# Kernel optimization log

Hardware: AMD Instinct MI355X
Metric: run time of the kernel (lower is better)

## Reference

```python
import jax, jax.numpy as jnp
import numpy as np

D_MODEL = 1024
H = 16
D_K = 64
D_V = 64
NEG_INF = -1e9
LN_EPS = 1e-5


def setup_inputs() -> dict:
    key = jax.random.key(0)
    ks = jax.random.split(key, 7)
    B, S = 4, 2048
    scale = 1.0 / np.sqrt(D_MODEL)
    return {
        "Q": jax.random.normal(ks[0], (B, S, D_MODEL), jnp.float32),
        "K": jax.random.normal(ks[1], (B, S, D_MODEL), jnp.float32),
        "V": jax.random.normal(ks[2], (B, S, D_MODEL), jnp.float32),
        "W_Q": jax.random.normal(ks[3], (D_MODEL, D_K * H), jnp.float32) * scale,
        "W_K": jax.random.normal(ks[4], (D_MODEL, D_K * H), jnp.float32) * scale,
        "W_V": jax.random.normal(ks[5], (D_MODEL, D_V * H), jnp.float32) * scale,
        "W_O": jax.random.normal(ks[6], (D_V * H, D_MODEL), jnp.float32) * scale,
        "ln_gamma": jnp.ones((D_MODEL,), jnp.float32),
        "ln_beta": jnp.zeros((D_MODEL,), jnp.float32),
    }


def reference(Q, K, V, W_Q, W_K, W_V, W_O, ln_gamma, ln_beta):
    B, Lq, _ = Q.shape
    Lk = K.shape[1]
    # projections, split into heads: [B, H, L, d]
    Qh = (Q @ W_Q).reshape(B, Lq, H, D_K).transpose(0, 2, 1, 3)
    Kh = (K @ W_K).reshape(B, Lk, H, D_K).transpose(0, 2, 1, 3)
    Vh = (V @ W_V).reshape(B, Lk, H, D_V).transpose(0, 2, 1, 3)
    # scaled dot-product scores [B, H, Lq, Lk]
    scores = jnp.einsum("bhqd,bhkd->bhqk", Qh, Kh) / jnp.sqrt(jnp.float32(D_K))
    # causal mask: upper triangle (excl. diagonal) gets -1e9 added
    mask = jnp.triu(jnp.full((Lq, Lk), NEG_INF, jnp.float32), k=1)
    scores = scores + mask
    attn = jax.nn.softmax(scores, axis=-1)
    ctx = jnp.einsum("bhqk,bhkd->bhqd", attn, Vh)
    ctx = ctx.transpose(0, 2, 1, 3).reshape(B, Lq, H * D_V)
    out = ctx @ W_O
    # residual + layernorm
    x = Q + out
    mu = jnp.mean(x, axis=-1, keepdims=True)
    var = jnp.mean(jnp.square(x - mu), axis=-1, keepdims=True)
    return (x - mu) * jax.lax.rsqrt(var + LN_EPS) * ln_gamma + ln_beta
```

## Files before the change

### kernel.cpp

```cpp
#include <hip/hip_runtime.h>
#include <cstdint>
#include <cstddef>

#define DM  1024
#define SEQ 2048
#define BATCH 4
#define NH  16
#define DH  64
#define QKVS 3072

typedef __bf16 bf16_t;
typedef __bf16 bf16x8 __attribute__((ext_vector_type(8)));
typedef __bf16 bf16x4 __attribute__((ext_vector_type(4)));
typedef float  f32x4  __attribute__((ext_vector_type(4)));

#define MFMA16(a, b, c) __builtin_amdgcn_mfma_f32_16x16x32_bf16((a), (b), (c), 0, 0, 0)

#define CS 0.18033688f

#define ASYNC_COPY16(gsrc, ldst)                                                   \
  __builtin_amdgcn_global_load_lds(                                                \
      (__attribute__((address_space(1))) void*)(gsrc),                             \
      (__attribute__((address_space(3))) void*)(ldst), 16, 0, 0)

#define NCVT (3 * BATCH * SEQ * DM / 4 / 256)

__global__ __launch_bounds__(256) void prep_kernel(const float* __restrict__ Q,
                                                   const float* __restrict__ K,
                                                   const float* __restrict__ V,
                                                   const float* __restrict__ W0,
                                                   const float* __restrict__ W1,
                                                   const float* __restrict__ W2,
                                                   const float* __restrict__ W3,
                                                   bf16_t* __restrict__ Qb,
                                                   bf16_t* __restrict__ Kb,
                                                   bf16_t* __restrict__ Vb,
                                                   bf16_t* __restrict__ WTall) {
  __shared__ float tile[32][33];
  const int bid = blockIdx.x;
  if (bid < NCVT) {
    const int n4 = BATCH * SEQ * DM / 4;
    int i = bid * 256 + threadIdx.x;
    const float* src; bf16_t* dst; int j;
    if (i < n4)           { src = Q; dst = Qb; j = i; }
    else if (i < 2 * n4)  { src = K; dst = Kb; j = i - n4; }
    else                  { src = V; dst = Vb; j = i - 2 * n4; }
    float4 v = ((const float4*)src)[j];
    bf16x4 o;
    o[0] = (bf16_t)v.x; o[1] = (bf16_t)v.y; o[2] = (bf16_t)v.z; o[3] = (bf16_t)v.w;
    *(bf16x4*)(dst + (size_t)j * 4) = o;
    return;
  }
  const int wb = bid - NCVT;
  const int widx = wb >> 10, wid = wb & 1023;
  const float* W = (widx == 0) ? W0 : (widx == 1) ? W1 : (widx == 2) ? W2 : W3;
  bf16_t* WT = WTall + (size_t)widx * DM * DM;
  const int bn = wid & 31, bk = wid >> 5;
  const int tx = threadIdx.x & 31, ty = threadIdx.x >> 5;
#pragma unroll
  for (int r = 0; r < 4; ++r)
    tile[ty + r * 8][tx] = W[(size_t)(bk * 32 + ty + r * 8) * DM + bn * 32 + tx];
  __syncthreads();
#pragma unroll
  for (int r = 0; r < 4; ++r)
    WT[(size_t)(bn * 32 + ty + r * 8) * DM + bk * 32 + tx] = (bf16_t)tile[tx][ty + r * 8];
}

template <typename OutT>
__global__ __launch_bounds__(256) void gemm_bt_kernel(const bf16_t* __restrict__ A0,
                                                      const bf16_t* __restrict__ A1,
                                                      const bf16_t* __restrict__ A2,
                                                      const bf16_t* __restrict__ BT,
                                                      OutT* __restrict__ C,
                                                      int K, int ldc,
                                                      float qscale, int qcols) {
  __shared__ bf16_t As[128 * 32];
  __shared__ bf16_t Bs[128 * 32];
  const int tid = threadIdx.x;
  const int wv = tid >> 6, lane = tid & 63;
  const int lo = lane & 15, quad = lane >> 4;

  const int bid = blockIdx.x;
  const int xcd = bid & 7;
  const int rid = bid >> 3;
  const int m0 = (xcd * 8 + (rid & 7)) * 128;
  const int n0 = (rid >> 3) * 128;
  const int wm = wv & 1, wn = wv >> 1;

  const bf16_t* A = (n0 < 1024) ? A0 : (n0 < 2048) ? A1 : A2;
  const float sc = (n0 < qcols) ? qscale : 1.0f;

  f32x4 acc[4][4] = {};

  const int srow = wv * 32 + (lane >> 2);
  const int scol = (lane & 3) * 8;
  const bf16_t* Ag = A + (size_t)(m0 + srow) * K + scol;
  const bf16_t* Bg = BT + (size_t)(n0 + srow) * K + scol;
  bf16_t* Asl = As + (wv * 32) * 32;
  bf16_t* Bsl = Bs + (wv * 32) * 32;

  for (int k0 = 0; k0 < K; k0 += 32) {
    __syncthreads();
    ASYNC_COPY16(Ag + k0, Asl);
    ASYNC_COPY16(Ag + k0 + (size_t)16 * K, Asl + 16 * 32);
    ASYNC_COPY16(Bg + k0, Bsl);
    ASYNC_COPY16(Bg + k0 + (size_t)16 * K, Bsl + 16 * 32);
    __syncthreads();

    bf16x8 af[4], bfr[4];
#pragma unroll
    for (int t = 0; t < 4; ++t) {
      af[t]  = *(const bf16x8*)(As + (wm * 64 + t * 16 + lo) * 32 + quad * 8);
      bfr[t] = *(const bf16x8*)(Bs + (wn * 64 + t * 16 + lo) * 32 + quad * 8);
    }
#pragma unroll
    for (int mt = 0; mt < 4; ++mt)
#pragma unroll
      for (int nt = 0; nt < 4; ++nt)
        acc[mt][nt] = MFMA16(af[mt], bfr[nt], acc[mt][nt]);
  }

#pragma unroll
  for (int mt = 0; mt < 4; ++mt)
#pragma unroll
    for (int nt = 0; nt < 4; ++nt)
#pragma unroll
      for (int r = 0; r < 4; ++r) {
        const int m = m0 + wm * 64 + mt * 16 + quad * 4 + r;
        const int n = n0 + wn * 64 + nt * 16 + lo;
        C[(size_t)m * ldc + n] = (OutT)(acc[mt][nt][r] * sc);
      }
}

__global__ __launch_bounds__(256) void vtrans_kernel(const bf16_t* __restrict__ QKV,
                                                     bf16_t* __restrict__ Vt) {
  __shared__ bf16_t tile[64][72];
  const int bh = blockIdx.x >> 5, jt = blockIdx.x & 31;
  const int b = bh >> 4, h = bh & 15;
  const bf16_t* src = QKV + ((size_t)(b * SEQ + jt * 64)) * QKVS + 2048 + h * DH;
  const int jr = threadIdx.x >> 3, c8 = (threadIdx.x & 7) * 8;
#pragma unroll
  for (int it = 0; it < 2; ++it) {
    const int j = jr + it * 32;
    *(bf16x8*)(&tile[j][c8]) = *(const bf16x8*)(src + (size_t)j * QKVS + c8);
  }
  __syncthreads();
  const int d = threadIdx.x >> 2, jc = (threadIdx.x & 3) * 16;
  bf16x8 o0, o1;
#pragma unroll
  for (int u = 0; u < 8; ++u) { o0[u] = tile[jc + u][d]; o1[u] = tile[jc + 8 + u][d]; }
  bf16_t* dst = Vt + ((size_t)(bh * 64 + d)) * SEQ + jt * 64 + jc;
  *(bf16x8*)(dst) = o0;
  *(bf16x8*)(dst + 8) = o1;
}

__global__ __launch_bounds__(256) void attn_kernel(const bf16_t* __restrict__ QKV,
                                                   const bf16_t* __restrict__ Vt,
                                                   bf16_t* __restrict__ ctx) {
  __shared__ bf16_t Ks[2][64 * 64];
  __shared__ bf16_t Vs[2][64 * 64];
  __shared__ bf16_t Ps[4][16 * 64];
  const int tid = threadIdx.x;
  const int wv = tid >> 6, lane = tid & 63;
  const int lo = lane & 15, quad = lane >> 4;
  const int bh = blockIdx.x & 63;
  const int pid = blockIdx.x >> 6;
  const int b = bh >> 4, h = bh & 15;

  const bf16_t* Qg = QKV + ((size_t)b * SEQ) * QKVS + h * DH;
  const bf16_t* Kg = QKV + ((size_t)b * SEQ) * QKVS + 1024 + h * DH;
  const bf16_t* Vg = Vt + ((size_t)(bh * DH)) * SEQ;

  const int U0 = wv * 128 + lane, U1 = U0 + 64;
  const int r0 = U0 >> 3, cg0 = (U0 & 7) ^ (r0 & 7);
  const int r1 = U1 >> 3, cg1 = (U1 & 7) ^ (r1 & 7);

  bf16_t* Pw = &Ps[wv][0];

  for (int half = 0; half < 2; ++half) {
    const int qblk = half ? (31 - pid) : pid;
    const int qw0 = qblk * 64 + wv * 16;
    const int qg = qw0 + lo;

    const bf16_t* Qb = Qg + ((size_t)(qw0 + lo)) * QKVS + quad * 8;
    const bf16x8 aQ0 = *(const bf16x8*)(Qb);
    const bf16x8 aQ1 = *(const bf16x8*)(Qb + 32);

    f32x4 O[4] = {};
    float l_run = 0.0f;

    __syncthreads();
    ASYNC_COPY16(Kg + (size_t)r0 * QKVS + cg0 * 8, Ks[0] + (wv * 2 + 0) * 512);
    ASYNC_COPY16(Kg + (size_t)r1 * QKVS + cg1 * 8, Ks[0] + (wv * 2 + 1) * 512);
    ASYNC_COPY16(Vg + (size_t)r0 * SEQ + cg0 * 8, Vs[0] + (wv * 2 + 0) * 512);
    ASYNC_COPY16(Vg + (size_t)r1 * SEQ + cg1 * 8, Vs[0] + (wv * 2 + 1) * 512);

    for (int jt = 0; jt <= qblk; ++jt) {
      const int cur = jt & 1;
      __syncthreads();
      if (jt < qblk) {
        const int j1 = (jt + 1) * 64;
        ASYNC_COPY16(Kg + (size_t)(j1 + r0) * QKVS + cg0 * 8, Ks[cur ^ 1] + (wv * 2 + 0) * 512);
        ASYNC_COPY16(Kg + (size_t)(j1 + r1) * QKVS + cg1 * 8, Ks[cur ^ 1] + (wv * 2 + 1) * 512);
        ASYNC_COPY16(Vg + (size_t)r0 * SEQ + j1 + cg0 * 8, Vs[cur ^ 1] + (wv * 2 + 0) * 512);
        ASYNC_COPY16(Vg + (size_t)r1 * SEQ + j1 + cg1 * 8, Vs[cur ^ 1] + (wv * 2 + 1) * 512);
      }

      const int j0 = jt * 64;
      f32x4 st[4];
#pragma unroll
      for (int mt = 0; mt < 4; ++mt) {
        const int row = mt * 16 + lo;
        const bf16x8 k0 = *(const bf16x8*)(Ks[cur] + row * 64 + ((quad ^ (row & 7)) * 8));
        const bf16x8 k1 = *(const bf16x8*)(Ks[cur] + row * 64 + (((4 + quad) ^ (row & 7)) * 8));
        f32x4 s = {};
        s = MFMA16(k0, aQ0, s);
        s = MFMA16(k1, aQ1, s);
        st[mt] = s;
      }

      float lsum = 0.0f;
      const bool diag = (jt == qblk);
#pragma unroll
      for (int mt = 0; mt < 4; ++mt) {
        bf16x4 pk;
#pragma unroll
        for (int r = 0; r < 4; ++r) {
          float s = st[mt][r];
          if (diag && (j0 + mt * 16 + quad * 4 + r > qg)) s = -1e30f;
          const float p = __builtin_amdgcn_exp2f(s);
          lsum += p;
          pk[r] = (bf16_t)p;
        }
        const int sp = (mt * 2 + (quad >> 1)) ^ (lo & 7);
        *(bf16x4*)(Pw + lo * 64 + sp * 8 + (quad & 1) * 4) = pk;
      }
      lsum += __shfl_xor(lsum, 16);
      lsum += __shfl_xor(lsum, 32);
      l_run += lsum;

      __asm__ volatile("s_waitcnt lgkmcnt(0)" ::: "memory");
      const bf16x8 p0 = *(const bf16x8*)(Pw + lo * 64 + ((quad ^ (lo & 7)) * 8));
      const bf16x8 p1 = *(const bf16x8*)(Pw + lo * 64 + (((4 + quad) ^ (lo & 7)) * 8));
#pragma unroll
      for (int nt = 0; nt < 4; ++nt) {
        const int row = nt * 16 + lo;
        const bf16x8 v0 = *(const bf16x8*)(Vs[cur] + row * 64 + ((quad ^ (row & 7)) * 8));
        const bf16x8 v1 = *(const bf16x8*)(Vs[cur] + row * 64 + (((4 + quad) ^ (row & 7)) * 8));
        O[nt] = MFMA16(p0, v0, O[nt]);
        O[nt] = MFMA16(p1, v1, O[nt]);
      }
    }

    float inv[4];
#pragma unroll
    for (int r = 0; r < 4; ++r) inv[r] = 1.0f / __shfl(l_run, quad * 4 + r);
    bf16_t* outp = ctx + ((size_t)(b * SEQ + qw0 + quad * 4)) * DM + h * DH + lo;
#pragma unroll
    for (int r = 0; r < 4; ++r)
#pragma unroll
      for (int nt = 0; nt < 4; ++nt)
        outp[(size_t)r * DM + nt * 16] = (bf16_t)(O[nt][r] * inv[r]);
  }
}

__global__ __launch_bounds__(256) void ln_kernel(const float* __restrict__ Qin,
                                                 const bf16_t* __restrict__ Y,
                                                 const float* __restrict__ gamma,
                                                 const float* __restrict__ beta,
                                                 float* __restrict__ out) {
  const int row = blockIdx.x, t = threadIdx.x;
  const float4 a = ((const float4*)(Qin + (size_t)row * DM))[t];
  const bf16x4 yv = ((const bf16x4*)(Y + (size_t)row * DM))[t];
  const float x0 = a.x + (float)yv[0], x1 = a.y + (float)yv[1];
  const float x2 = a.z + (float)yv[2], x3 = a.w + (float)yv[3];
  float s  = x0 + x1 + x2 + x3;
  float ss = x0 * x0 + x1 * x1 + x2 * x2 + x3 * x3;
#pragma unroll
  for (int off = 1; off < 64; off <<= 1) { s += __shfl_xor(s, off); ss += __shfl_xor(ss, off); }
  __shared__ float red[8];
  const int wv = t >> 6, lane = t & 63;
  if (lane == 0) { red[wv * 2] = s; red[wv * 2 + 1] = ss; }
  __syncthreads();
  s  = red[0] + red[2] + red[4] + red[6];
  ss = red[1] + red[3] + red[5] + red[7];
  const float mu  = s * (1.0f / DM);
  const float var = ss * (1.0f / DM) - mu * mu;
  const float rstd = rsqrtf(var + 1e-5f);
  const float4 g  = ((const float4*)gamma)[t];
  const float4 be = ((const float4*)beta)[t];
  float4 o;
  o.x = (x0 - mu) * rstd * g.x + be.x;
  o.y = (x1 - mu) * rstd * g.y + be.y;
  o.z = (x2 - mu) * rstd * g.z + be.z;
  o.w = (x3 - mu) * rstd * g.w + be.w;
  ((float4*)(out + (size_t)row * DM))[t] = o;
}

extern "C" void kernel_launch(void* const* d_in, const int* in_sizes, int n_in,
                              void* d_out, int out_size, void* d_ws, size_t ws_size,
                              hipStream_t stream) {
  const float* Q     = (const float*)d_in[0];
  const float* K     = (const float*)d_in[1];
  const float* V     = (const float*)d_in[2];
  const float* W_Q   = (const float*)d_in[3];
  const float* W_K   = (const float*)d_in[4];
  const float* W_V   = (const float*)d_in[5];
  const float* W_O   = (const float*)d_in[6];
  const float* gamma = (const float*)d_in[7];
  const float* beta  = (const float*)d_in[8];
  float* out = (float*)d_out;

  char* ws = (char*)d_ws;
  const size_t SZB = (size_t)BATCH * SEQ * DM * 2;
  const size_t WTB = (size_t)DM * DM * 2;
  bf16_t* Qb    = (bf16_t*)(ws);
  bf16_t* Kb    = (bf16_t*)(ws + SZB);
  bf16_t* Vb    = (bf16_t*)(ws + 2 * SZB);
  bf16_t* Yb    = (bf16_t*)(ws);
  bf16_t* WTall = (bf16_t*)(ws + 3 * SZB);
  char* p2 = ws + 3 * SZB + 4 * WTB;
  bf16_t* QKV = (bf16_t*)(p2);
  bf16_t* Vtr = (bf16_t*)(p2 + 3 * SZB);
  bf16_t* ctx = (bf16_t*)(p2 + 4 * SZB);

  prep_kernel<<<NCVT + 4096, 256, 0, stream>>>(Q, K, V, W_Q, W_K, W_V, W_O,
                                               Qb, Kb, Vb, WTall);

  gemm_bt_kernel<bf16_t><<<(QKVS / 128) * (BATCH * SEQ / 128), 256, 0, stream>>>(
      Qb, Kb, Vb, WTall, QKV, DM, QKVS, CS, 1024);

  vtrans_kernel<<<BATCH * NH * (SEQ / 64), 256, 0, stream>>>(QKV, Vtr);

  attn_kernel<<<64 * 16, 256, 0, stream>>>(QKV, Vtr, ctx);

  gemm_bt_kernel<bf16_t><<<(DM / 128) * (BATCH * SEQ / 128), 256, 0, stream>>>(
      ctx, ctx, ctx, WTall + (size_t)3 * DM * DM, Yb, DM, DM, 1.0f, 0);
  ln_kernel<<<BATCH * SEQ, 256, 0, stream>>>(Q, Yb, gamma, beta, out);
}
```

Measured before the change: 337.8 us.

## Fuse V transpose into QKV GEMM epilogue and double-buffer GEMM LDS loads

The QKV projection GEMM now writes the V columns straight into the transposed per-head layout through an LDS-staged, swizzled epilogue. This removes the separate vtrans kernel and the round trip of V through global memory, and the QKV buffer shrinks to Q and K only. The GEMM main loop also double-buffers its A/B tiles in LDS, so the next K-slice is prefetched while MFMAs run, cutting one barrier per iteration. The cost is twice the LDS per block, which may lower occupancy, plus extra epilogue complexity.

Result: faster. 316.3 us (-6.4%).

```diff
diff --git a/kernel.cpp b/kernel.cpp
--- a/kernel.cpp
+++ b/kernel.cpp
@@ -7,7 +7,7 @@
 #define BATCH 4
 #define NH  16
 #define DH  64
-#define QKVS 3072
+#define QKS 2048
 
 typedef __bf16 bf16_t;
 typedef __bf16 bf16x8 __attribute__((ext_vector_type(8)));
@@ -66,16 +66,15 @@
     WT[(size_t)(bn * 32 + ty + r * 8) * DM + bk * 32 + tx] = (bf16_t)tile[tx][ty + r * 8];
 }
 
-template <typename OutT>
 __global__ __launch_bounds__(256) void gemm_bt_kernel(const bf16_t* __restrict__ A0,
                                                       const bf16_t* __restrict__ A1,
                                                       const bf16_t* __restrict__ A2,
                                                       const bf16_t* __restrict__ BT,
-                                                      OutT* __restrict__ C,
+                                                      bf16_t* __restrict__ C,
+                                                      bf16_t* __restrict__ Vtr,
                                                       int K, int ldc,
                                                       float qscale, int qcols) {
-  __shared__ bf16_t As[128 * 32];
-  __shared__ bf16_t Bs[128 * 32];
+  __shared__ bf16_t Sh[4][128 * 32];
   const int tid = threadIdx.x;
   const int wv = tid >> 6, lane = tid & 63;
   const int lo = lane & 15, quad = lane >> 4;
@@ -96,22 +95,30 @@
   const int scol = (lane & 3) * 8;
   const bf16_t* Ag = A + (size_t)(m0 + srow) * K + scol;
   const bf16_t* Bg = BT + (size_t)(n0 + srow) * K + scol;
-  bf16_t* Asl = As + (wv * 32) * 32;
-  bf16_t* Bsl = Bs + (wv * 32) * 32;
-
-  for (int k0 = 0; k0 < K; k0 += 32) {
+  const int lds_off = (wv * 32) * 32;
+
+  ASYNC_COPY16(Ag, Sh[0] + lds_off);
+  ASYNC_COPY16(Ag + (size_t)16 * K, Sh[0] + lds_off + 16 * 32);
+  ASYNC_COPY16(Bg, Sh[2] + lds_off);
+  ASYNC_COPY16(Bg + (size_t)16 * K, Sh[2] + lds_off + 16 * 32);
+
+  const int kiters = K >> 5;
+  for (int ki = 0; ki < kiters; ++ki) {
+    const int cur = ki & 1;
     __syncthreads();
-    ASYNC_COPY16(Ag + k0, Asl);
-    ASYNC_COPY16(Ag + k0 + (size_t)16 * K, Asl + 16 * 32);
-    ASYNC_COPY16(Bg + k0, Bsl);
-    ASYNC_COPY16(Bg + k0 + (size_t)16 * K, Bsl + 16 * 32);
-    __syncthreads();
+    if (ki + 1 < kiters) {
+      const int k1 = (ki + 1) << 5;
+      ASYNC_COPY16(Ag + k1, Sh[cur ^ 1] + lds_off);
+      ASYNC_COPY16(Ag + k1 + (size_t)16 * K, Sh[cur ^ 1] + lds_off + 16 * 32);
+      ASYNC_COPY16(Bg + k1, Sh[2 + (cur ^ 1)] + lds_off);
+      ASYNC_COPY16(Bg + k1 + (size_t)16 * K, Sh[2 + (cur ^ 1)] + lds_off + 16 * 32);
+    }
 
     bf16x8 af[4], bfr[4];
 #pragma unroll
     for (int t = 0; t < 4; ++t) {
-      af[t]  = *(const bf16x8*)(As + (wm * 64 + t * 16 + lo) * 32 + quad * 8);
-      bfr[t] = *(const bf16x8*)(Bs + (wn * 64 + t * 16 + lo) * 32 + quad * 8);
+      af[t]  = *(const bf16x8*)(Sh[cur] + (wm * 64 + t * 16 + lo) * 32 + quad * 8);
+      bfr[t] = *(const bf16x8*)(Sh[2 + cur] + (wn * 64 + t * 16 + lo) * 32 + quad * 8);
     }
 #pragma unroll
     for (int mt = 0; mt < 4; ++mt)
@@ -120,6 +127,38 @@
         acc[mt][nt] = MFMA16(af[mt], bfr[nt], acc[mt][nt]);
   }
 
+  __syncthreads();
+
+  if (Vtr != nullptr && n0 >= 2048) {
+    bf16_t* Tw = &Sh[wv][0];
+#pragma unroll
+    for (int nt = 0; nt < 4; ++nt) {
+      const int row = nt * 16 + lo;
+#pragma unroll
+      for (int mt = 0; mt < 4; ++mt) {
+        const int cb = mt * 16 + quad * 4;
+        bf16x4 pk;
+#pragma unroll
+        for (int r = 0; r < 4; ++r) pk[r] = (bf16_t)acc[mt][nt][r];
+        *(bf16x4*)(Tw + row * 64 + (((cb >> 3) ^ (row & 7)) * 8) + (cb & 7)) = pk;
+      }
+    }
+    __asm__ volatile("s_waitcnt lgkmcnt(0)" ::: "memory");
+    const int h  = ((n0 - 2048) >> 6) + wn;
+    const int mg = m0 + wm * 64;
+    const int b  = mg >> 11;
+    const int s0 = mg & (SEQ - 1);
+    const int dr = lane >> 3, ck = lane & 7;
+    bf16_t* vbase = Vtr + ((size_t)((b * NH + h) * DH)) * SEQ + s0;
+#pragma unroll
+    for (int pass = 0; pass < 8; ++pass) {
+      const int d = pass * 8 + dr;
+      const bf16x8 vv = *(const bf16x8*)(Tw + d * 64 + ((ck ^ (d & 7)) * 8));
+      *(bf16x8*)(vbase + (size_t)d * SEQ + ck * 8) = vv;
+    }
+    return;
+  }
+
 #pragma unroll
   for (int mt = 0; mt < 4; ++mt)
 #pragma unroll
@@ -128,30 +167,8 @@
       for (int r = 0; r < 4; ++r) {
         const int m = m0 + wm * 64 + mt * 16 + quad * 4 + r;
         const int n = n0 + wn * 64 + nt * 16 + lo;
-        C[(size_t)m * ldc + n] = (OutT)(acc[mt][nt][r] * sc);
-      }
-}
-
-__global__ __launch_bounds__(256) void vtrans_kernel(const bf16_t* __restrict__ QKV,
-                                                     bf16_t* __restrict__ Vt) {
-  __shared__ bf16_t tile[64][72];
-  const int bh = blockIdx.x >> 5, jt = blockIdx.x & 31;
-  const int b = bh >> 4, h = bh & 15;
-  const bf16_t* src = QKV + ((size_t)(b * SEQ + jt * 64)) * QKVS + 2048 + h * DH;
-  const int jr = threadIdx.x >> 3, c8 = (threadIdx.x & 7) * 8;
-#pragma unroll
-  for (int it = 0; it < 2; ++it) {
-    const int j = jr + it * 32;
-    *(bf16x8*)(&tile[j][c8]) = *(const bf16x8*)(src + (size_t)j * QKVS + c8);
-  }
-  __syncthreads();
-  const int d = threadIdx.x >> 2, jc = (threadIdx.x & 3) * 16;
-  bf16x8 o0, o1;
-#pragma unroll
-  for (int u = 0; u < 8; ++u) { o0[u] = tile[jc + u][d]; o1[u] = tile[jc + 8 + u][d]; }
-  bf16_t* dst = Vt + ((size_t)(bh * 64 + d)) * SEQ + jt * 64 + jc;
-  *(bf16x8*)(dst) = o0;
-  *(bf16x8*)(dst + 8) = o1;
+        C[(size_t)m * ldc + n] = (bf16_t)(acc[mt][nt][r] * sc);
+      }
 }
 
 __global__ __launch_bounds__(256) void attn_kernel(const bf16_t* __restrict__ QKV,
@@ -167,8 +184,8 @@
   const int pid = blockIdx.x >> 6;
   const int b = bh >> 4, h = bh & 15;
 
-  const bf16_t* Qg = QKV + ((size_t)b * SEQ) * QKVS + h * DH;
-  const bf16_t* Kg = QKV + ((size_t)b * SEQ) * QKVS + 1024 + h * DH;
+  const bf16_t* Qg = QKV + ((size_t)b * SEQ) * QKS + h * DH;
+  const bf16_t* Kg = QKV + ((size_t)b * SEQ) * QKS + 1024 + h * DH;
   const bf16_t* Vg = Vt + ((size_t)(bh * DH)) * SEQ;
 
   const int U0 = wv * 128 + lane, U1 = U0 + 64;
@@ -182,7 +199,7 @@
     const int qw0 = qblk * 64 + wv * 16;
     const int qg = qw0 + lo;
 
-    const bf16_t* Qb = Qg + ((size_t)(qw0 + lo)) * QKVS + quad * 8;
+    const bf16_t* Qb = Qg + ((size_t)(qw0 + lo)) * QKS + quad * 8;
     const bf16x8 aQ0 = *(const bf16x8*)(Qb);
     const bf16x8 aQ1 = *(const bf16x8*)(Qb + 32);
 
@@ -190,8 +207,8 @@
     float l_run = 0.0f;
 
     __syncthreads();
-    ASYNC_COPY16(Kg + (size_t)r0 * QKVS + cg0 * 8, Ks[0] + (wv * 2 + 0) * 512);
-    ASYNC_COPY16(Kg + (size_t)r1 * QKVS + cg1 * 8, Ks[0] + (wv * 2 + 1) * 512);
+    ASYNC_COPY16(Kg + (size_t)r0 * QKS + cg0 * 8, Ks[0] + (wv * 2 + 0) * 512);
+    ASYNC_COPY16(Kg + (size_t)r1 * QKS + cg1 * 8, Ks[0] + (wv * 2 + 1) * 512);
     ASYNC_COPY16(Vg + (size_t)r0 * SEQ + cg0 * 8, Vs[0] + (wv * 2 + 0) * 512);
     ASYNC_COPY16(Vg + (size_t)r1 * SEQ + cg1 * 8, Vs[0] + (wv * 2 + 1) * 512);
 
@@ -200,8 +217,8 @@
       __syncthreads();
       if (jt < qblk) {
         const int j1 = (jt + 1) * 64;
-        ASYNC_COPY16(Kg + (size_t)(j1 + r0) * QKVS + cg0 * 8, Ks[cur ^ 1] + (wv * 2 + 0) * 512);
-        ASYNC_COPY16(Kg + (size_t)(j1 + r1) * QKVS + cg1 * 8, Ks[cur ^ 1] + (wv * 2 + 1) * 512);
+        ASYNC_COPY16(Kg + (size_t)(j1 + r0) * QKS + cg0 * 8, Ks[cur ^ 1] + (wv * 2 + 0) * 512);
+        ASYNC_COPY16(Kg + (size_t)(j1 + r1) * QKS + cg1 * 8, Ks[cur ^ 1] + (wv * 2 + 1) * 512);
         ASYNC_COPY16(Vg + (size_t)r0 * SEQ + j1 + cg0 * 8, Vs[cur ^ 1] + (wv * 2 + 0) * 512);
         ASYNC_COPY16(Vg + (size_t)r1 * SEQ + j1 + cg1 * 8, Vs[cur ^ 1] + (wv * 2 + 1) * 512);
       }
@@ -321,20 +338,18 @@
   bf16_t* WTall = (bf16_t*)(ws + 3 * SZB);
   char* p2 = ws + 3 * SZB + 4 * WTB;
   bf16_t* QKV = (bf16_t*)(p2);
-  bf16_t* Vtr = (bf16_t*)(p2 + 3 * SZB);
-  bf16_t* ctx = (bf16_t*)(p2 + 4 * SZB);
+  bf16_t* Vtr = (bf16_t*)(p2 + 2 * SZB);
+  bf16_t* ctx = (bf16_t*)(p2 + 3 * SZB);
 
   prep_kernel<<<NCVT + 4096, 256, 0, stream>>>(Q, K, V, W_Q, W_K, W_V, W_O,
                                                Qb, Kb, Vb, WTall);
 
-  gemm_bt_kernel<bf16_t><<<(QKVS / 128) * (BATCH * SEQ / 128), 256, 0, stream>>>(
-      Qb, Kb, Vb, WTall, QKV, DM, QKVS, CS, 1024);
-
-  vtrans_kernel<<<BATCH * NH * (SEQ / 64), 256, 0, stream>>>(QKV, Vtr);
+  gemm_bt_kernel<<<(3072 / 128) * (BATCH * SEQ / 128), 256, 0, stream>>>(
+      Qb, Kb, Vb, WTall, QKV, Vtr, DM, QKS, CS, 1024);
 
   attn_kernel<<<64 * 16, 256, 0, stream>>>(QKV, Vtr, ctx);
 
-  gemm_bt_kernel<bf16_t><<<(DM / 128) * (BATCH * SEQ / 128), 256, 0, stream>>>(
-      ctx, ctx, ctx, WTall + (size_t)3 * DM * DM, Yb, DM, DM, 1.0f, 0);
+  gemm_bt_kernel<<<(DM / 128) * (BATCH * SEQ / 128), 256, 0, stream>>>(
+      ctx, ctx, ctx, WTall + (size_t)3 * DM * DM, Yb, nullptr, DM, DM, 1.0f, 0);
   ln_kernel<<<BATCH * SEQ, 256, 0, stream>>>(Q, Yb, gamma, beta, out);
 }
```
